# Kernel optimization log

Measured on AMD Instinct MI355X. Metric: run time of the kernel, lower is better.

Reference implementation:

```python
import jax, jax.numpy as jnp
import numpy as np

N, E = 50000, 800000
IN_DIM, EDGE_DIM, HID, OUT_DIM, L = 128, 16, 64, 8, 4
MSG_EPS = 1e-7  # GENConv eps added to relu(msg)


def layer_norm(x, g, b, eps=1e-5):
    mu = x.mean(-1, keepdims=True)
    var = ((x - mu) ** 2).mean(-1, keepdims=True)
    return (x - mu) * jax.lax.rsqrt(var + eps) * g + b


def segment_softmax(logits, seg, num_segments):
    # numerically stable softmax over edges grouped by destination node
    m = jax.ops.segment_max(logits, seg, num_segments=num_segments)
    m = jnp.where(jnp.isfinite(m), m, 0.0)
    e = jnp.exp(logits - m[seg])
    s = jax.ops.segment_sum(e, seg, num_segments=num_segments)
    return e / (s[seg] + 1e-16)


def gen_conv(x, src, dst, ea, t, W1, b1, g1, be1, W2, b2):
    # GENConv: message = relu(x_j + e_ij) + eps, softmax-aggregate by dst, add root, MLP [h->2h->h]
    msg = jax.nn.relu(x[src] + ea) + MSG_EPS          # [E, H]
    alpha = segment_softmax(msg * t, dst, x.shape[0]) # [E, H]
    agg = jax.ops.segment_sum(msg * alpha, dst, num_segments=x.shape[0])  # [N, H]
    h = agg + x
    h = jax.nn.relu(layer_norm(h @ W1 + b1, g1, be1))  # [N, 2H]
    return h @ W2 + b2                                 # [N, H]


def setup_inputs() -> dict:
    key = jax.random.key(0)
    ks = jax.random.split(key, 16)
    sc = 0.05
    inp = {
        "x": jax.random.normal(ks[0], (N, IN_DIM), jnp.float32),
        "edge_attr": jax.random.normal(ks[1], (E, EDGE_DIM), jnp.float32),
        "node_W": jax.random.normal(ks[2], (IN_DIM, HID), jnp.float32) * sc,
        "node_b": jnp.zeros((HID,), jnp.float32),
        "edge_W": jax.random.normal(ks[3], (EDGE_DIM, HID), jnp.float32) * sc,
        "edge_b": jnp.zeros((HID,), jnp.float32),
        "conv_t": jnp.ones((L,), jnp.float32),
        "conv_W1": jax.random.normal(ks[4], (L, HID, 2 * HID), jnp.float32) * sc,
        "conv_b1": jnp.zeros((L, 2 * HID), jnp.float32),
        "conv_g1": jnp.ones((L, 2 * HID), jnp.float32),
        "conv_be1": jnp.zeros((L, 2 * HID), jnp.float32),
        "conv_W2": jax.random.normal(ks[5], (L, 2 * HID, HID), jnp.float32) * sc,
        "conv_b2": jnp.zeros((L, HID), jnp.float32),
        "ln_g": jnp.ones((L, HID), jnp.float32),
        "ln_b": jnp.zeros((L, HID), jnp.float32),
        "lin_W": jax.random.normal(ks[6], (HID, OUT_DIM), jnp.float32) * sc,
        "lin_b": jnp.zeros((OUT_DIM,), jnp.float32),
        "edge_index": jax.random.randint(ks[7], (2, E), 0, N, jnp.int64),
    }
    return inp


def reference(x, edge_attr, node_W, node_b, edge_W, edge_b,
              conv_t, conv_W1, conv_b1, conv_g1, conv_be1, conv_W2, conv_b2,
              ln_g, ln_b, lin_W, lin_b, edge_index):
    src, dst = edge_index[0], edge_index[1]  # flow: source_to_target
    h = x @ node_W + node_b
    ea = edge_attr @ edge_W + edge_b
    # first layer: conv only (DeeperGCN applies layers[0].conv directly)
    h = gen_conv(h, src, dst, ea, conv_t[0], conv_W1[0], conv_b1[0],
                 conv_g1[0], conv_be1[0], conv_W2[0], conv_b2[0])
    # res+ blocks: x + conv(dropout(relu(norm(x)))); dropout inactive (eval)
    for i in range(1, L):
        z = jax.nn.relu(layer_norm(h, ln_g[i], ln_b[i]))
        h = h + gen_conv(z, src, dst, ea, conv_t[i], conv_W1[i], conv_b1[i],
                         conv_g1[i], conv_be1[i], conv_W2[i], conv_b2[i])
    h = jax.nn.relu(layer_norm(h, ln_g[0], ln_b[0]))
    return h @ lin_W + lin_b
```

## Files before the change

kernel.cpp:

```cpp
#include <hip/hip_runtime.h>
#include <hip/hip_fp16.h>

#define N_NODES 50000
#define N_EDGES 800000
#define IN_DIM  128
#define EDGE_DIM 16
#define HID     64
#define HID2    128
#define OUT_DIM 8
#define N_LAYERS 4
#define NBUCK   391
#define CCHUNK  4096
#define CBLOCKS 196

typedef _Float16 half8 __attribute__((ext_vector_type(8)));
typedef float floatx4 __attribute__((ext_vector_type(4)));

__global__ __launch_bounds__(256, 4) void chist_kernel(
    const int* __restrict__ dsts, int* __restrict__ ccnt)
{
    __shared__ int lh[NBUCK];
    for (int i = threadIdx.x; i < NBUCK; i += 256) lh[i] = 0;
    __syncthreads();
    const int base = blockIdx.x * CCHUNK;
#pragma unroll
    for (int i = 0; i < 16; ++i) {
        const int e = base + i * 256 + threadIdx.x;
        if (e < N_EDGES) atomicAdd(&lh[dsts[e] >> 7], 1);
    }
    __syncthreads();
    for (int i = threadIdx.x; i < NBUCK; i += 256)
        if (lh[i]) atomicAdd(&ccnt[i], lh[i]);
}

__global__ __launch_bounds__(256, 1) void cscan_kernel(
    const int* __restrict__ ccnt, int* __restrict__ coff, int* __restrict__ ccur)
{
    __shared__ int part[512];
    const int t = threadIdx.x;
    part[t]       = (t < NBUCK)       ? ccnt[t]       : 0;
    part[t + 256] = (t + 256 < NBUCK) ? ccnt[t + 256] : 0;
    __syncthreads();
    for (int off = 1; off < 512; off <<= 1) {
        const int v0 = (t >= off) ? part[t - off] : 0;
        const int v1 = (t + 256 >= off) ? part[t + 256 - off] : 0;
        __syncthreads();
        part[t] += v0; part[t + 256] += v1;
        __syncthreads();
    }
    if (t < NBUCK) { const int ex = (t > 0) ? part[t - 1] : 0; coff[t] = ex; ccur[t] = ex; }
    const int i2 = t + 256;
    if (i2 < NBUCK) { coff[i2] = part[i2 - 1]; ccur[i2] = part[i2 - 1]; }
    if (t == 0) coff[NBUCK] = part[NBUCK - 1];
}

__global__ __launch_bounds__(256, 4) void cscatter_kernel(
    const int* __restrict__ srcs, const int* __restrict__ dsts,
    int* __restrict__ ccur, uint2* __restrict__ tmp)
{
    __shared__ int lh[NBUCK], lbase[NBUCK], lrank[NBUCK];
    for (int i = threadIdx.x; i < NBUCK; i += 256) { lh[i] = 0; lrank[i] = 0; }
    __syncthreads();
    const int base = blockIdx.x * CCHUNK;
    int myd[16], mys[16];
#pragma unroll
    for (int i = 0; i < 16; ++i) {
        const int e = base + i * 256 + threadIdx.x;
        if (e < N_EDGES) {
            myd[i] = dsts[e]; mys[i] = srcs[e];
            atomicAdd(&lh[myd[i] >> 7], 1);
        } else myd[i] = -1;
    }
    __syncthreads();
    for (int i = threadIdx.x; i < NBUCK; i += 256) {
        const int c = lh[i];
        lbase[i] = c ? atomicAdd(&ccur[i], c) : 0;
    }
    __syncthreads();
#pragma unroll
    for (int i = 0; i < 16; ++i) {
        if (myd[i] >= 0) {
            const int e = base + i * 256 + threadIdx.x;
            const int b = myd[i] >> 7;
            const int r = atomicAdd(&lrank[b], 1);
            tmp[lbase[b] + r] =
                make_uint2((unsigned)mys[i] | ((unsigned)myd[i] << 16),
                           (unsigned)e);
        }
    }
}

__global__ __launch_bounds__(256, 1) void fsort_kernel(
    const uint2* __restrict__ tmp, const int* __restrict__ coff,
    unsigned* __restrict__ sd2, int* __restrict__ eid)
{
    __shared__ uint2 ebuf[4096];
    __shared__ int lh[128], lsc[128];
    const int b = blockIdx.x;
    const int lo = coff[b];
    const int cnt = coff[b + 1] - lo;
    if (threadIdx.x < 128) lh[threadIdx.x] = 0;
    __syncthreads();
    for (int i = threadIdx.x; i < cnt; i += 256) {
        const uint2 v = tmp[lo + i];
        ebuf[i] = v;
        atomicAdd(&lh[(int)(v.x >> 16) - b * 128], 1);
    }
    __syncthreads();
    if (threadIdx.x < 128) lsc[threadIdx.x] = lh[threadIdx.x];
    __syncthreads();
    for (int off = 1; off < 128; off <<= 1) {
        int v = 0;
        if (threadIdx.x < 128 && threadIdx.x >= off) v = lsc[threadIdx.x - off];
        __syncthreads();
        if (threadIdx.x < 128) lsc[threadIdx.x] += v;
        __syncthreads();
    }
    if (threadIdx.x < 128) lh[threadIdx.x] = lsc[threadIdx.x] - lh[threadIdx.x];
    __syncthreads();
    for (int i = threadIdx.x; i < cnt; i += 256) {
        const uint2 v = ebuf[i];
        const int d = (int)(v.x >> 16) - b * 128;
        const int pos = atomicAdd(&lh[d], 1);
        sd2[lo + pos] = v.x;
        eid[lo + pos] = (int)v.y;
    }
}

__global__ __launch_bounds__(256, 2) void node_proj_kernel(
    const float* __restrict__ x, const float* __restrict__ W,
    const float* __restrict__ b, float* __restrict__ h, __half* __restrict__ zh)
{
    __shared__ float xs[4][IN_DIM];
    const int c = threadIdx.x & 63;
    const int local_n = threadIdx.x >> 6;
    float w[IN_DIM];
#pragma unroll
    for (int k = 0; k < IN_DIM; ++k) w[k] = W[k * HID + c];
    const float bias = b[c];

    for (int base = blockIdx.x * 4; base < N_NODES; base += gridDim.x * 4) {
        __syncthreads();
#pragma unroll
        for (int i = 0; i < 2; ++i) {
            int idx = threadIdx.x + i * 256;
            int nn = idx >> 7, kk = idx & 127;
            xs[nn][kk] = x[(base + nn) * IN_DIM + kk];
        }
        __syncthreads();
        const int n = base + local_n;
        float acc = bias;
#pragma unroll
        for (int k4 = 0; k4 < IN_DIM / 4; ++k4) {
            float4 xv = ((const float4*)xs[local_n])[k4];
            acc = fmaf(xv.x, w[k4 * 4 + 0], acc);
            acc = fmaf(xv.y, w[k4 * 4 + 1], acc);
            acc = fmaf(xv.z, w[k4 * 4 + 2], acc);
            acc = fmaf(xv.w, w[k4 * 4 + 3], acc);
        }
        h[n * HID + c] = acc;
        zh[n * HID + c] = __float2half(acc);
    }
}

__global__ __launch_bounds__(256, 4) void edge_emb_kernel(
    const float* __restrict__ ea, const float* __restrict__ W,
    const float* __restrict__ b, const int* __restrict__ eid,
    __half* __restrict__ eah)
{
    __shared__ __half lds_t[4][16 * HID];
    const int lane = threadIdx.x & 63;
    const int waveid = threadIdx.x >> 6;
    const int wave = (blockIdx.x * 256 + threadIdx.x) >> 6;
    const int nwaves = gridDim.x * 4;
    const int m = lane & 15, q = lane >> 4;
    const int NT = N_EDGES / 16;

    half8 bf[4];
#pragma unroll
    for (int blk = 0; blk < 4; ++blk) {
#pragma unroll
        for (int i = 0; i < 8; ++i) {
            const int k = q * 8 + i;
            bf[blk][i] = (k < EDGE_DIM)
                ? (_Float16)W[k * HID + blk * 16 + m] : (_Float16)0.f;
        }
    }
    float bv[4];
#pragma unroll
    for (int blk = 0; blk < 4; ++blk) bv[blk] = b[blk * 16 + m];

    const int ed = lane >> 3, ch = lane & 7;

    for (int tile = wave; tile < NT; tile += nwaves) {
        const int e0 = tile * 16;
        const int eidx = eid[e0 + m];
        half8 af;
#pragma unroll
        for (int i = 0; i < 8; ++i) af[i] = (_Float16)0.f;
        if (q < 2) {
            const float4* ap =
                (const float4*)(ea + (size_t)eidx * EDGE_DIM + q * 8);
            const float4 lo = ap[0];
            const float4 hi = ap[1];
            af[0] = (_Float16)lo.x; af[1] = (_Float16)lo.y;
            af[2] = (_Float16)lo.z; af[3] = (_Float16)lo.w;
            af[4] = (_Float16)hi.x; af[5] = (_Float16)hi.y;
            af[6] = (_Float16)hi.z; af[7] = (_Float16)hi.w;
        }
        floatx4 c[4];
#pragma unroll
        for (int blk = 0; blk < 4; ++blk) {
            floatx4 cin = {bv[blk], bv[blk], bv[blk], bv[blk]};
            c[blk] = __builtin_amdgcn_mfma_f32_16x16x32_f16(
                af, bf[blk], cin, 0, 0, 0);
        }
#pragma unroll
        for (int blk = 0; blk < 4; ++blk)
#pragma unroll
            for (int r = 0; r < 4; ++r)
                lds_t[waveid][(q * 4 + r) * HID + blk * 16 + m] =
                    __float2half(c[blk][r]);
        const float4 v0 =
            *(const float4*)&lds_t[waveid][ed * HID + ch * 8];
        const float4 v1 =
            *(const float4*)&lds_t[waveid][(8 + ed) * HID + ch * 8];
        ((float4*)(eah + (size_t)(e0 + ed) * HID))[ch] = v0;
        ((float4*)(eah + (size_t)(e0 + 8 + ed) * HID))[ch] = v1;
    }
}

__global__ __launch_bounds__(256, 4) void edge_agg_kernel(
    const __half* __restrict__ zh, const __half* __restrict__ eah,
    const unsigned* __restrict__ sd2,
    const float* __restrict__ conv_t, int layer,
    float* __restrict__ p, float* __restrict__ s)
{
    const int lane = threadIdx.x & 63;
    const int wave = (blockIdx.x * 256 + threadIdx.x) >> 6;
    const int nwaves = gridDim.x * 4;
    const float t2 = conv_t[layer] * 1.4426950408889634f;
    const int NT = N_EDGES / 64;

    const _Float16* zf = (const _Float16*)zh;
    const _Float16* ef = (const _Float16*)eah;

    for (int tile = wave; tile < NT; tile += nwaves) {
        const int e0 = tile * 64;
        const unsigned sdv = sd2[e0 + lane];
        const int sv = (int)(sdv & 0xffffu);
        const int dv = (int)(sdv >> 16);
        const int pv = __shfl_up(dv, 1, 64);
        const unsigned long long bmask = __ballot(dv != pv) & ~1ull;
        const _Float16* erow = ef + (size_t)e0 * HID + lane;

        _Float16 za[8], ez[8], zb[8], eb[8];
#pragma unroll
        for (int k = 0; k < 8; ++k) {
            const int a = __builtin_amdgcn_readlane(sv, k);
            za[k] = (zf + (size_t)a * HID)[lane];
            ez[k] = erow[(size_t)k * HID];
        }

        float S = 0.f, P = 0.f;
        int cur = __builtin_amdgcn_readlane(dv, 0);
#pragma unroll
        for (int g = 0; g < 8; ++g) {
            if (g < 7) {
#pragma unroll
                for (int k = 0; k < 8; ++k) {
                    const int a = __builtin_amdgcn_readlane(sv, (g + 1) * 8 + k);
                    zb[k] = (zf + (size_t)a * HID)[lane];
                    eb[k] = erow[(size_t)((g + 1) * 8 + k) * HID];
                }
            }
#pragma unroll
            for (int k = 0; k < 8; ++k) {
                const int j = g * 8 + k;
                if (bmask & (1ull << j)) {
                    unsafeAtomicAdd(&s[(size_t)cur * HID + lane], S);
                    unsafeAtomicAdd(&p[(size_t)cur * HID + lane], P);
                    S = 0.f; P = 0.f;
                    cur = __builtin_amdgcn_readlane(dv, j);
                }
                _Float16 mh = za[k] + ez[k];
                mh = mh > (_Float16)0.f ? mh : (_Float16)0.f;
                const float m = (float)mh + 1e-7f;
                const float xx = __builtin_amdgcn_exp2f(m * t2);
                S += xx;
                P = fmaf(m, xx, P);
            }
            if (g < 7) {
#pragma unroll
                for (int k = 0; k < 8; ++k) { za[k] = zb[k]; ez[k] = eb[k]; }
            }
        }
        unsafeAtomicAdd(&s[(size_t)cur * HID + lane], S);
        unsafeAtomicAdd(&p[(size_t)cur * HID + lane], P);
    }
}

__global__ __launch_bounds__(256, 2) void node_mm1_kernel(
    float* __restrict__ p, float* __restrict__ s,
    const __half* __restrict__ zh,
    const float* __restrict__ W1, const float* __restrict__ b1,
    const float* __restrict__ g1, const float* __restrict__ be1,
    __half* __restrict__ vh)
{
    __shared__ float hs[2][HID];
    __shared__ float red[2][2][2];
    const int j = threadIdx.x & 127;
    const int local_n = threadIdx.x >> 7;
    const int wavehalf = (threadIdx.x >> 6) & 1;
    float w[HID];
#pragma unroll
    for (int k = 0; k < HID; ++k) w[k] = W1[k * HID2 + j];
    const float bias = b1[j];
    const float g = g1[j];
    const float be = be1[j];

    for (int base = blockIdx.x * 2; base < N_NODES; base += gridDim.x * 2) {
        __syncthreads();
        if (threadIdx.x < 128) {
            int nn = threadIdx.x >> 6, c = threadIdx.x & 63;
            int idx = (base + nn) * HID + c;
            hs[nn][c] = p[idx] / (s[idx] + 1e-16f) + __half2float(zh[idx]);
            p[idx] = 0.f;
            s[idx] = 0.f;
        }
        __syncthreads();
        const int n = base + local_n;
        float u = bias;
#pragma unroll
        for (int k4 = 0; k4 < HID / 4; ++k4) {
            float4 hv = ((const float4*)hs[local_n])[k4];
            u = fmaf(hv.x, w[k4 * 4 + 0], u);
            u = fmaf(hv.y, w[k4 * 4 + 1], u);
            u = fmaf(hv.z, w[k4 * 4 + 2], u);
            u = fmaf(hv.w, w[k4 * 4 + 3], u);
        }
        float ps_ = u;
#pragma unroll
        for (int o = 1; o < 64; o <<= 1) ps_ += __shfl_xor(ps_, o, 64);
        if ((threadIdx.x & 63) == 0) red[local_n][0][wavehalf] = ps_;
        __syncthreads();
        const float mu = (red[local_n][0][0] + red[local_n][0][1]) * (1.f / 128.f);
        const float d = u - mu;
        float q = d * d;
#pragma unroll
        for (int o = 1; o < 64; o <<= 1) q += __shfl_xor(q, o, 64);
        if ((threadIdx.x & 63) == 0) red[local_n][1][wavehalf] = q;
        __syncthreads();
        const float var = (red[local_n][1][0] + red[local_n][1][1]) * (1.f / 128.f);
        const float y = d * rsqrtf(var + 1e-5f) * g + be;
        vh[(size_t)n * HID2 + j] = __float2half(y > 0.f ? y : 0.f);
    }
}

__global__ __launch_bounds__(256, 2) void node_mm2_kernel(
    const __half* __restrict__ vh,
    const float* __restrict__ W2, const float* __restrict__ b2,
    const float* __restrict__ lng, const float* __restrict__ lnb,
    float* __restrict__ h, __half* __restrict__ zh, int residual)
{
    __shared__ float vs[4][HID2];
    const int c = threadIdx.x & 63;
    const int local_n = threadIdx.x >> 6;
    float w[HID2];
#pragma unroll
    for (int k = 0; k < HID2; ++k) w[k] = W2[k * HID + c];
    const float bias = b2[c];
    const float g = lng[c];
    const float be = lnb[c];

    for (int base = blockIdx.x * 4; base < N_NODES; base += gridDim.x * 4) {
        __syncthreads();
        {
            const __half2* vp = (const __half2*)(vh + (size_t)base * HID2);
            const float2 f = __half22float2(vp[threadIdx.x]);
            const int nn = threadIdx.x >> 6, kk = (threadIdx.x & 63) * 2;
            vs[nn][kk] = f.x;
            vs[nn][kk + 1] = f.y;
        }
        __syncthreads();
        const int n = base + local_n;
        float acc = bias;
#pragma unroll
        for (int k4 = 0; k4 < HID2 / 4; ++k4) {
            float4 vv = ((const float4*)vs[local_n])[k4];
            acc = fmaf(vv.x, w[k4 * 4 + 0], acc);
            acc = fmaf(vv.y, w[k4 * 4 + 1], acc);
            acc = fmaf(vv.z, w[k4 * 4 + 2], acc);
            acc = fmaf(vv.w, w[k4 * 4 + 3], acc);
        }
        const float hn = residual ? (h[n * HID + c] + acc) : acc;
        h[n * HID + c] = hn;
        float ps_ = hn;
#pragma unroll
        for (int o = 1; o < 64; o <<= 1) ps_ += __shfl_xor(ps_, o, 64);
        const float mu = ps_ * (1.f / 64.f);
        const float d = hn - mu;
        float q = d * d;
#pragma unroll
        for (int o = 1; o < 64; o <<= 1) q += __shfl_xor(q, o, 64);
        const float var = q * (1.f / 64.f);
        const float y = d * rsqrtf(var + 1e-5f) * g + be;
        zh[n * HID + c] = __float2half(y > 0.f ? y : 0.f);
    }
}

__global__ __launch_bounds__(256, 4) void final_kernel(
    const __half* __restrict__ zh, const float* __restrict__ Wl,
    const float* __restrict__ bl, float* __restrict__ out)
{
    __shared__ float wl[HID * OUT_DIM];
    for (int i = threadIdx.x; i < HID * OUT_DIM; i += 256) wl[i] = Wl[i];
    __syncthreads();
    const int total = N_NODES * OUT_DIM;
    for (int idx = blockIdx.x * 256 + threadIdx.x; idx < total;
         idx += gridDim.x * 256) {
        const int n = idx >> 3, o = idx & 7;
        const __half2* zp = (const __half2*)(zh + (size_t)n * HID);
        float acc = bl[o];
#pragma unroll
        for (int k2 = 0; k2 < HID / 2; ++k2) {
            const float2 f = __half22float2(zp[k2]);
            acc = fmaf(f.x, wl[(k2 * 2 + 0) * OUT_DIM + o], acc);
            acc = fmaf(f.y, wl[(k2 * 2 + 1) * OUT_DIM + o], acc);
        }
        out[idx] = acc;
    }
}

extern "C" void kernel_launch(void* const* d_in, const int* in_sizes, int n_in,
                              void* d_out, int out_size, void* d_ws, size_t ws_size,
                              hipStream_t stream)
{
    const float* x         = (const float*)d_in[0];
    const float* edge_attr = (const float*)d_in[1];
    const float* node_W    = (const float*)d_in[2];
    const float* node_b    = (const float*)d_in[3];
    const float* edge_W    = (const float*)d_in[4];
    const float* edge_b    = (const float*)d_in[5];
    const float* conv_t    = (const float*)d_in[6];
    const float* conv_W1   = (const float*)d_in[7];
    const float* conv_b1   = (const float*)d_in[8];
    const float* conv_g1   = (const float*)d_in[9];
    const float* conv_be1  = (const float*)d_in[10];
    const float* conv_W2   = (const float*)d_in[11];
    const float* conv_b2   = (const float*)d_in[12];
    const float* ln_g      = (const float*)d_in[13];
    const float* ln_b      = (const float*)d_in[14];
    const float* lin_W     = (const float*)d_in[15];
    const float* lin_b     = (const float*)d_in[16];
    const int*   edge_index= (const int*)d_in[17];
    const int*   srcs = edge_index;
    const int*   dsts = edge_index + N_EDGES;
    float* out = (float*)d_out;

    float* h   = (float*)d_ws;
    float* p   = h   + N_NODES * HID;
    float* s   = p   + N_NODES * HID;
    __half* vh  = (__half*)(s + N_NODES * HID);
    __half* zh  = vh + (size_t)N_NODES * HID2;
    __half* eah = zh + (size_t)N_NODES * HID;
    uint2* tmp  = (uint2*)(eah + (size_t)N_EDGES * HID);
    unsigned* sd2 = (unsigned*)(tmp + N_EDGES);
    int* eid    = (int*)(sd2 + N_EDGES);
    int* ccnt   = eid + N_EDGES;
    int* coff   = ccnt + NBUCK;
    int* ccur   = coff + NBUCK + 1;

    hipMemsetAsync(ccnt, 0, (size_t)NBUCK * sizeof(int), stream);
    chist_kernel<<<CBLOCKS, 256, 0, stream>>>(dsts, ccnt);
    cscan_kernel<<<1, 256, 0, stream>>>(ccnt, coff, ccur);
    cscatter_kernel<<<CBLOCKS, 256, 0, stream>>>(srcs, dsts, ccur, tmp);
    fsort_kernel<<<NBUCK, 256, 0, stream>>>(tmp, coff, sd2, eid);

    node_proj_kernel<<<2048, 256, 0, stream>>>(x, node_W, node_b, h, zh);
    edge_emb_kernel<<<3125, 256, 0, stream>>>(edge_attr, edge_W, edge_b, eid, eah);

    hipMemsetAsync(p, 0, (size_t)2 * N_NODES * HID * sizeof(float), stream);

    for (int layer = 0; layer < N_LAYERS; ++layer) {
        edge_agg_kernel<<<3125, 256, 0, stream>>>(zh, eah, sd2,
                                                  conv_t, layer, p, s);
        node_mm1_kernel<<<2048, 256, 0, stream>>>(
            p, s, zh,
            conv_W1 + (size_t)layer * HID * HID2, conv_b1 + layer * HID2,
            conv_g1 + layer * HID2, conv_be1 + layer * HID2, vh);
        const float* gz = (layer < N_LAYERS - 1) ? (ln_g + (layer + 1) * HID) : ln_g;
        const float* bz = (layer < N_LAYERS - 1) ? (ln_b + (layer + 1) * HID) : ln_b;
        node_mm2_kernel<<<2048, 256, 0, stream>>>(
            vh, conv_W2 + (size_t)layer * HID2 * HID, conv_b2 + layer * HID,
            gz, bz, h, zh, layer > 0 ? 1 : 0);
    }
    final_kernel<<<1024, 256, 0, stream>>>(zh, lin_W, lin_b, out);
}
```

Before: 750.2 us.

## Rewrite node MLP kernels as wave-per-node with readlane broadcasts

```diff
diff --git a/kernel.cpp b/kernel.cpp
--- a/kernel.cpp
+++ b/kernel.cpp
@@ -15,6 +15,10 @@
 
 typedef _Float16 half8 __attribute__((ext_vector_type(8)));
 typedef float floatx4 __attribute__((ext_vector_type(4)));
+
+static __device__ __forceinline__ float bcast(float v, int l) {
+    return __uint_as_float(__builtin_amdgcn_readlane(__float_as_uint(v), l));
+}
 
 __global__ __launch_bounds__(256, 4) void chist_kernel(
     const int* __restrict__ dsts, int* __restrict__ ccnt)
@@ -300,112 +304,118 @@
     }
 }
 
-__global__ __launch_bounds__(256, 2) void node_mm1_kernel(
+__global__ __launch_bounds__(256, 3) void node_mm1_kernel(
     float* __restrict__ p, float* __restrict__ s,
     const __half* __restrict__ zh,
     const float* __restrict__ W1, const float* __restrict__ b1,
     const float* __restrict__ g1, const float* __restrict__ be1,
     __half* __restrict__ vh)
 {
-    __shared__ float hs[2][HID];
-    __shared__ float red[2][2][2];
-    const int j = threadIdx.x & 127;
-    const int local_n = threadIdx.x >> 7;
-    const int wavehalf = (threadIdx.x >> 6) & 1;
-    float w[HID];
-#pragma unroll
-    for (int k = 0; k < HID; ++k) w[k] = W1[k * HID2 + j];
-    const float bias = b1[j];
-    const float g = g1[j];
-    const float be = be1[j];
-
-    for (int base = blockIdx.x * 2; base < N_NODES; base += gridDim.x * 2) {
-        __syncthreads();
-        if (threadIdx.x < 128) {
-            int nn = threadIdx.x >> 6, c = threadIdx.x & 63;
-            int idx = (base + nn) * HID + c;
-            hs[nn][c] = p[idx] / (s[idx] + 1e-16f) + __half2float(zh[idx]);
-            p[idx] = 0.f;
-            s[idx] = 0.f;
-        }
-        __syncthreads();
-        const int n = base + local_n;
-        float u = bias;
-#pragma unroll
-        for (int k4 = 0; k4 < HID / 4; ++k4) {
-            float4 hv = ((const float4*)hs[local_n])[k4];
-            u = fmaf(hv.x, w[k4 * 4 + 0], u);
-            u = fmaf(hv.y, w[k4 * 4 + 1], u);
-            u = fmaf(hv.z, w[k4 * 4 + 2], u);
-            u = fmaf(hv.w, w[k4 * 4 + 3], u);
-        }
-        float ps_ = u;
-#pragma unroll
-        for (int o = 1; o < 64; o <<= 1) ps_ += __shfl_xor(ps_, o, 64);
-        if ((threadIdx.x & 63) == 0) red[local_n][0][wavehalf] = ps_;
-        __syncthreads();
-        const float mu = (red[local_n][0][0] + red[local_n][0][1]) * (1.f / 128.f);
-        const float d = u - mu;
-        float q = d * d;
+    const int lane = threadIdx.x & 63;
+    const int wave = (blockIdx.x * 256 + threadIdx.x) >> 6;
+    const int nwaves = gridDim.x * 4;
+
+    float wa[HID], wb[HID];
+#pragma unroll
+    for (int k = 0; k < HID; ++k) {
+        wa[k] = W1[k * HID2 + lane];
+        wb[k] = W1[k * HID2 + 64 + lane];
+    }
+    const float ba = b1[lane],  bb = b1[64 + lane];
+    const float ga = g1[lane],  gb = g1[64 + lane];
+    const float ca = be1[lane], cb = be1[64 + lane];
+
+    for (int n = wave; n < N_NODES; n += nwaves) {
+        const int idx = n * HID + lane;
+        const float pv = p[idx];
+        const float sv = s[idx];
+        const float zv = __half2float(zh[idx]);
+        p[idx] = 0.f;
+        s[idx] = 0.f;
+        const float hv = pv / (sv + 1e-16f) + zv;
+
+        float a0 = 0.f, a1 = 0.f, c0 = 0.f, c1 = 0.f;
+#pragma unroll
+        for (int k = 0; k < 32; ++k) {
+            const float x0 = bcast(hv, k);
+            const float x1 = bcast(hv, k + 32);
+            a0 = fmaf(x0, wa[k], a0);
+            c0 = fmaf(x0, wb[k], c0);
+            a1 = fmaf(x1, wa[k + 32], a1);
+            c1 = fmaf(x1, wb[k + 32], c1);
+        }
+        const float ua = (a0 + a1) + ba;
+        const float ub = (c0 + c1) + bb;
+
+        float sum = ua + ub;
+#pragma unroll
+        for (int o = 1; o < 64; o <<= 1) sum += __shfl_xor(sum, o, 64);
+        const float mu = sum * (1.f / 128.f);
+        const float da = ua - mu, db = ub - mu;
+        float q = fmaf(da, da, db * db);
 #pragma unroll
         for (int o = 1; o < 64; o <<= 1) q += __shfl_xor(q, o, 64);
-        if ((threadIdx.x & 63) == 0) red[local_n][1][wavehalf] = q;
-        __syncthreads();
-        const float var = (red[local_n][1][0] + red[local_n][1][1]) * (1.f / 128.f);
-        const float y = d * rsqrtf(var + 1e-5f) * g + be;
-        vh[(size_t)n * HID2 + j] = __float2half(y > 0.f ? y : 0.f);
-    }
-}
-
-__global__ __launch_bounds__(256, 2) void node_mm2_kernel(
+        const float rstd = rsqrtf(q * (1.f / 128.f) + 1e-5f);
+        const float ya = da * rstd * ga + ca;
+        const float yb = db * rstd * gb + cb;
+        vh[(size_t)n * HID2 + lane]      = __float2half(ya > 0.f ? ya : 0.f);
+        vh[(size_t)n * HID2 + 64 + lane] = __float2half(yb > 0.f ? yb : 0.f);
+    }
+}
+
+__global__ __launch_bounds__(256, 3) void node_mm2_kernel(
     const __half* __restrict__ vh,
     const float* __restrict__ W2, const float* __restrict__ b2,
     const float* __restrict__ lng, const float* __restrict__ lnb,
     float* __restrict__ h, __half* __restrict__ zh, int residual)
 {
-    __shared__ float vs[4][HID2];
-    const int c = threadIdx.x & 63;
-    const int local_n = threadIdx.x >> 6;
-    float w[HID2];
-#pragma unroll
-    for (int k = 0; k < HID2; ++k) w[k] = W2[k * HID + c];
-    const float bias = b2[c];
-    const float g = lng[c];
-    const float be = lnb[c];
-
-    for (int base = blockIdx.x * 4; base < N_NODES; base += gridDim.x * 4) {
-        __syncthreads();
-        {
-            const __half2* vp = (const __half2*)(vh + (size_t)base * HID2);
-            const float2 f = __half22float2(vp[threadIdx.x]);
-            const int nn = threadIdx.x >> 6, kk = (threadIdx.x & 63) * 2;
-            vs[nn][kk] = f.x;
-            vs[nn][kk + 1] = f.y;
-        }
-        __syncthreads();
-        const int n = base + local_n;
-        float acc = bias;
-#pragma unroll
-        for (int k4 = 0; k4 < HID2 / 4; ++k4) {
-            float4 vv = ((const float4*)vs[local_n])[k4];
-            acc = fmaf(vv.x, w[k4 * 4 + 0], acc);
-            acc = fmaf(vv.y, w[k4 * 4 + 1], acc);
-            acc = fmaf(vv.z, w[k4 * 4 + 2], acc);
-            acc = fmaf(vv.w, w[k4 * 4 + 3], acc);
-        }
-        const float hn = residual ? (h[n * HID + c] + acc) : acc;
-        h[n * HID + c] = hn;
-        float ps_ = hn;
-#pragma unroll
-        for (int o = 1; o < 64; o <<= 1) ps_ += __shfl_xor(ps_, o, 64);
-        const float mu = ps_ * (1.f / 64.f);
+    const int lane = threadIdx.x & 63;
+    const int wave = (blockIdx.x * 256 + threadIdx.x) >> 6;
+    const int nwaves = gridDim.x * 4;
+
+    float wa[HID2 / 2], wb[HID2 / 2];
+#pragma unroll
+    for (int k = 0; k < HID2 / 2; ++k) {
+        wa[k] = W2[k * HID + lane];
+        wb[k] = W2[(k + 64) * HID + lane];
+    }
+    const float bias = b2[lane];
+    const float g = lng[lane];
+    const float be = lnb[lane];
+
+    for (int n = wave; n < N_NODES; n += nwaves) {
+        const float f0 = __half2float(vh[(size_t)n * HID2 + lane]);
+        const float f1 = __half2float(vh[(size_t)n * HID2 + 64 + lane]);
+
+        float a0 = 0.f, a1 = 0.f, c0 = 0.f, c1 = 0.f;
+#pragma unroll
+        for (int k = 0; k < 32; ++k) {
+            const float x0 = bcast(f0, k);
+            const float x1 = bcast(f0, k + 32);
+            const float x2 = bcast(f1, k);
+            const float x3 = bcast(f1, k + 32);
+            a0 = fmaf(x0, wa[k], a0);
+            a1 = fmaf(x1, wa[k + 32], a1);
+            c0 = fmaf(x2, wb[k], c0);
+            c1 = fmaf(x3, wb[k + 32], c1);
+        }
+        const float acc = (a0 + a1) + (c0 + c1) + bias;
+
+        const int idx = n * HID + lane;
+        const float hn = residual ? (h[idx] + acc) : acc;
+        h[idx] = hn;
+
+        float sum = hn;
+#pragma unroll
+        for (int o = 1; o < 64; o <<= 1) sum += __shfl_xor(sum, o, 64);
+        const float mu = sum * (1.f / 64.f);
         const float d = hn - mu;
         float q = d * d;
 #pragma unroll
         for (int o = 1; o < 64; o <<= 1) q += __shfl_xor(q, o, 64);
         const float var = q * (1.f / 64.f);
         const float y = d * rsqrtf(var + 1e-5f) * g + be;
-        zh[n * HID + c] = __float2half(y > 0.f ? y : 0.f);
+        zh[idx] = __float2half(y > 0.f ? y : 0.f);
     }
 }
 
```

Result: faster. 670.4 us (-10.6%).
